# Kernel tuning notes

Measured on AMD Instinct MI355X. Metric: run time of the kernel, lower is better.

Reference implementation:

```python
import jax, jax.numpy as jnp
import numpy as np

N_NODES = 100000

def setup_inputs() -> dict:
    key = jax.random.key(0)
    k1, k2, k3, k4, k5 = jax.random.split(key, 5)
    feat = jax.random.normal(k1, (N_NODES, 64), dtype=jnp.float32)
    # Xavier-uniform-ish linear params
    W = jax.random.normal(k2, (64, 64), dtype=jnp.float32) * 0.125
    b = jax.random.normal(k3, (64,), dtype=jnp.float32) * 0.01
    E = 1600000
    src = jax.random.randint(k4, (E,), 0, N_NODES, dtype=jnp.int32)
    dst = jax.random.randint(k5, (E,), 0, N_NODES, dtype=jnp.int32)
    return {"feat": feat, "W": W, "b": b, "src": src, "dst": dst}

def reference(feat, W, b, src, dst):
    # update_all(copy_u('feat'), sum): neighbor-sum aggregation (SpMM)
    # message on edge e = feat[src[e]]; reduce: sum into dst node
    agg = jax.ops.segment_sum(feat[src], dst, num_segments=feat.shape[0])  # [N, in_feats]
    # apply_nodes: linear + relu (torch Linear: x @ W.T + b)
    h = agg @ W.T + b
    return jax.nn.relu(h)
```

## Files before the change

kernel.cpp:

```cpp
#include <hip/hip_runtime.h>


__device__ __forceinline__ float bcast_lane(float x, int k) {
    return __uint_as_float(__builtin_amdgcn_readlane(__float_as_uint(x), k));
}


__global__ void k_build_chains(const int* __restrict__ src,
                               const int* __restrict__ dst,
                               int* __restrict__ head,
                               int2* __restrict__ nodes, int E) {
    int e = blockIdx.x * blockDim.x + threadIdx.x;
    if (e < E) {
        int d = dst[e];
        int s = src[e];
        int prev = atomicExch(&head[d], e);
        nodes[e] = make_int2(prev, s);
    }
}


__global__ void k_gather_chain_linear(const float* __restrict__ feat,
                                      const float* __restrict__ W,
                                      const float* __restrict__ b,
                                      const int* __restrict__ head,
                                      const int2* __restrict__ nodes,
                                      float* __restrict__ out, int N) {
    int lane = threadIdx.x & 63;
    int wid = (blockIdx.x * blockDim.x + threadIdx.x) >> 6;
    int nw = (gridDim.x * blockDim.x) >> 6;

    float4 w[16];
    const float4* Wv = (const float4*)(W + (lane << 6));
    #pragma unroll
    for (int q = 0; q < 16; ++q) w[q] = Wv[q];
    float bj = b[lane];

    for (int n = wid; n < N; n += nw) {
        float sum = 0.0f;
        int e = head[n];
        if (e >= 0) {
            int2 nd = nodes[e];
            float v = feat[(nd.y << 6) + lane];
            e = nd.x;
            while (e >= 0) {
                int2 nd2 = nodes[e];
                float v2 = feat[(nd2.y << 6) + lane];
                sum += v;
                v = v2;
                e = nd2.x;
            }
            sum += v;
        }

        float acc = bj;
        #pragma unroll
        for (int k = 0; k < 64; ++k)
            acc = fmaf(bcast_lane(sum, k), ((const float*)w)[k], acc);
        out[(n << 6) + lane] = fmaxf(acc, 0.0f);
    }
}


__global__ void gcn_scatter_kernel(const float* __restrict__ feat,
                                   const int* __restrict__ src,
                                   const int* __restrict__ dst,
                                   float* __restrict__ agg,
                                   int n_edges) {
    long long tid = (long long)blockIdx.x * blockDim.x + threadIdx.x;
    int e = (int)(tid >> 6);
    int f = (int)(tid & 63);
    if (e >= n_edges) return;
    atomicAdd(&agg[(long long)dst[e] * 64 + f], feat[(long long)src[e] * 64 + f]);
}

__global__ void gcn_linear_relu_kernel(const float* __restrict__ agg,
                                       const float* __restrict__ W,
                                       const float* __restrict__ b,
                                       float* __restrict__ out,
                                       int n_nodes) {
    __shared__ float Wt[64 * 65];
    __shared__ float bs[64];
    __shared__ float rows[4 * 64];
    int tid = threadIdx.x;
    #pragma unroll
    for (int it = 0; it < 16; ++it) {
        int idx = it * 256 + tid;
        Wt[(idx & 63) * 65 + (idx >> 6)] = W[idx];
    }
    if (tid < 64) bs[tid] = b[tid];
    __syncthreads();
    int li = tid >> 6, j = tid & 63;
    for (int r0 = blockIdx.x * 4; r0 < n_nodes; r0 += gridDim.x * 4) {
        int n = r0 + li;
        __syncthreads();
        if (n < n_nodes) rows[tid] = agg[(long long)n * 64 + j];
        __syncthreads();
        if (n < n_nodes) {
            float sum = bs[j];
            #pragma unroll
            for (int k = 0; k < 64; ++k)
                sum += rows[li * 64 + k] * Wt[k * 65 + j];
            out[(long long)n * 64 + j] = fmaxf(sum, 0.0f);
        }
    }
}

extern "C" void kernel_launch(void* const* d_in, const int* in_sizes, int n_in,
                              void* d_out, int out_size, void* d_ws, size_t ws_size,
                              hipStream_t stream) {
    const float* feat = (const float*)d_in[0];
    const float* W    = (const float*)d_in[1];
    const float* b    = (const float*)d_in[2];
    const int*   src  = (const int*)d_in[3];
    const int*   dst  = (const int*)d_in[4];
    float* out = (float*)d_out;

    int N = in_sizes[0] / 64;
    int E = in_sizes[3];

    size_t need = (size_t)N * sizeof(int) + (size_t)E * sizeof(int2);

    if (ws_size >= need) {
        int*  head  = (int*)d_ws;
        int2* nodes = (int2*)(head + N);

        hipMemsetAsync(head, 0xFF, (size_t)N * sizeof(int), stream);

        k_build_chains<<<(E + 255) / 256, 256, 0, stream>>>(src, dst, head, nodes, E);

        k_gather_chain_linear<<<2048, 256, 0, stream>>>(feat, W, b, head, nodes, out, N);
    } else {
        float* agg = out;
        hipMemsetAsync(agg, 0, (size_t)N * 64 * sizeof(float), stream);
        long long total = (long long)E * 64;
        gcn_scatter_kernel<<<(int)((total + 255) / 256), 256, 0, stream>>>(feat, src, dst, agg, E);
        gcn_linear_relu_kernel<<<1280, 256, 0, stream>>>(agg, W, b, out, N);
    }
}
```

Baseline: 334.8 us.

## Gather bf16 features and walk two node chains per wavefront

Adds a pre-pass that casts the feature matrix to bf16 so each edge gather reads half the bytes. The gather kernel now processes two destination nodes per wavefront and interleaves their linked-list chain walks, giving more independent memory requests in flight. It reuses the register-held weights for both linear outputs. The cost is an extra cast kernel plus workspace, and a loss of accuracy from bf16 rounding of the inputs before summation. It also drops the previous one-ahead prefetch of the next chain node.

New measurement: 429.4 us. 1.28x slower.

```diff
diff --git a/kernel.cpp b/kernel.cpp
--- a/kernel.cpp
+++ b/kernel.cpp
@@ -3,6 +3,29 @@
 
 __device__ __forceinline__ float bcast_lane(float x, int k) {
     return __uint_as_float(__builtin_amdgcn_readlane(__float_as_uint(x), k));
+}
+__device__ __forceinline__ float bf16_to_f32(unsigned short h) {
+    return __uint_as_float(((unsigned int)h) << 16);
+}
+__device__ __forceinline__ unsigned short f32_to_bf16_rne(float f) {
+    unsigned int x = __float_as_uint(f);
+    unsigned int r = x + 0x7fffu + ((x >> 16) & 1u);
+    return (unsigned short)(r >> 16);
+}
+
+
+__global__ void k_cast_bf16(const float* __restrict__ feat,
+                            unsigned short* __restrict__ featB, int total4) {
+    int i = blockIdx.x * blockDim.x + threadIdx.x;
+    if (i < total4) {
+        float4 v = ((const float4*)feat)[i];
+        ushort4 o;
+        o.x = f32_to_bf16_rne(v.x);
+        o.y = f32_to_bf16_rne(v.y);
+        o.z = f32_to_bf16_rne(v.z);
+        o.w = f32_to_bf16_rne(v.w);
+        ((ushort4*)featB)[i] = o;
+    }
 }
 
 
@@ -20,12 +43,12 @@
 }
 
 
-__global__ void k_gather_chain_linear(const float* __restrict__ feat,
-                                      const float* __restrict__ W,
-                                      const float* __restrict__ b,
-                                      const int* __restrict__ head,
-                                      const int2* __restrict__ nodes,
-                                      float* __restrict__ out, int N) {
+__global__ void k_gather2_chain_linear(const unsigned short* __restrict__ featB,
+                                       const float* __restrict__ W,
+                                       const float* __restrict__ b,
+                                       const int* __restrict__ head,
+                                       const int2* __restrict__ nodes,
+                                       float* __restrict__ out, int N) {
     int lane = threadIdx.x & 63;
     int wid = (blockIdx.x * blockDim.x + threadIdx.x) >> 6;
     int nw = (gridDim.x * blockDim.x) >> 6;
@@ -36,28 +59,35 @@
     for (int q = 0; q < 16; ++q) w[q] = Wv[q];
     float bj = b[lane];
 
-    for (int n = wid; n < N; n += nw) {
-        float sum = 0.0f;
-        int e = head[n];
-        if (e >= 0) {
-            int2 nd = nodes[e];
-            float v = feat[(nd.y << 6) + lane];
-            e = nd.x;
-            while (e >= 0) {
-                int2 nd2 = nodes[e];
-                float v2 = feat[(nd2.y << 6) + lane];
-                sum += v;
-                v = v2;
-                e = nd2.x;
+    for (int p = wid; (p << 1) < N; p += nw) {
+        int n0 = p << 1;
+        int n1 = n0 + 1;
+        float s0 = 0.0f, s1 = 0.0f;
+        int e0 = head[n0];
+        int e1 = (n1 < N) ? head[n1] : -1;
+
+        while (e0 >= 0 || e1 >= 0) {
+            if (e0 >= 0) {
+                int2 a = nodes[e0];
+                s0 += bf16_to_f32(featB[(a.y << 6) + lane]);
+                e0 = a.x;
             }
-            sum += v;
+            if (e1 >= 0) {
+                int2 a = nodes[e1];
+                s1 += bf16_to_f32(featB[(a.y << 6) + lane]);
+                e1 = a.x;
+            }
         }
 
-        float acc = bj;
+        float acc0 = bj, acc1 = bj;
         #pragma unroll
-        for (int k = 0; k < 64; ++k)
-            acc = fmaf(bcast_lane(sum, k), ((const float*)w)[k], acc);
-        out[(n << 6) + lane] = fmaxf(acc, 0.0f);
+        for (int k = 0; k < 64; ++k) {
+            float wk = ((const float*)w)[k];
+            acc0 = fmaf(bcast_lane(s0, k), wk, acc0);
+            acc1 = fmaf(bcast_lane(s1, k), wk, acc1);
+        }
+        out[(n0 << 6) + lane] = fmaxf(acc0, 0.0f);
+        if (n1 < N) out[(n1 << 6) + lane] = fmaxf(acc1, 0.0f);
     }
 }
 
@@ -119,17 +149,24 @@
     int N = in_sizes[0] / 64;
     int E = in_sizes[3];
 
-    size_t need = (size_t)N * sizeof(int) + (size_t)E * sizeof(int2);
+    size_t featB_bytes = (size_t)N * 64 * sizeof(unsigned short);
+    size_t head_bytes  = (size_t)N * sizeof(int);
+    size_t nodes_bytes = (size_t)E * sizeof(int2);
+    size_t need = featB_bytes + head_bytes + nodes_bytes;
 
     if (ws_size >= need) {
-        int*  head  = (int*)d_ws;
-        int2* nodes = (int2*)(head + N);
+        unsigned short* featB = (unsigned short*)d_ws;
+        int*  head  = (int*)((char*)d_ws + featB_bytes);
+        int2* nodes = (int2*)((char*)d_ws + featB_bytes + head_bytes);
 
-        hipMemsetAsync(head, 0xFF, (size_t)N * sizeof(int), stream);
+        int total4 = N * 16;
+        k_cast_bf16<<<(total4 + 255) / 256, 256, 0, stream>>>(feat, featB, total4);
+
+        hipMemsetAsync(head, 0xFF, head_bytes, stream);
 
         k_build_chains<<<(E + 255) / 256, 256, 0, stream>>>(src, dst, head, nodes, E);
 
-        k_gather_chain_linear<<<2048, 256, 0, stream>>>(feat, W, b, head, nodes, out, N);
+        k_gather2_chain_linear<<<2048, 256, 0, stream>>>(featB, W, b, head, nodes, out, N);
     } else {
         float* agg = out;
         hipMemsetAsync(agg, 0, (size_t)N * 64 * sizeof(float), stream);
```
